# Kernel optimization log

Hardware: AMD Instinct MI355X
Metric: run time of the kernel (lower is better)

Reference implementation:

```python
import jax, jax.numpy as jnp
import numpy as np

N = 50000
E = 800000
G = 64
H, C = 16, 4  # heads, out_channels per head; H*C = 64


def setup_inputs() -> dict:
    key = jax.random.key(0)
    ks = jax.random.split(key, 16)
    return {
        "x": jax.random.normal(ks[0], (N,), jnp.float32),
        "edge_index": jax.random.randint(ks[1], (2, E), 0, N),
        "edge_attr": jax.random.normal(ks[2], (E,), jnp.float32),
        "batch": jnp.sort(jax.random.randint(ks[3], (N,), 0, G)),
        # GATv2Conv(1 -> 4, heads=16, edge_dim=1, concat=True)
        "Wl": jax.random.normal(ks[4], (1, H * C), jnp.float32) * 0.5,
        "bl": jnp.full((H * C,), 0.01, jnp.float32),
        "Wr": jax.random.normal(ks[5], (1, H * C), jnp.float32) * 0.5,
        "br": jnp.full((H * C,), 0.01, jnp.float32),
        "We": jax.random.normal(ks[6], (1, H * C), jnp.float32) * 0.5,
        "att": jax.random.normal(ks[7], (H, C), jnp.float32) * 0.5,
        "gat_bias": jnp.zeros((H * C,), jnp.float32),
        # GraphNorm(64)
        "gn_w": jnp.ones((H * C,), jnp.float32),
        "gn_b": jnp.zeros((H * C,), jnp.float32),
        "gn_ms": jnp.ones((H * C,), jnp.float32),
        # SAGEConv(64 -> 64, mean aggr, root weight)
        "sage_Wl": jax.random.normal(ks[8], (H * C, 64), jnp.float32) * 0.125,
        "sage_bl": jnp.full((64,), 0.01, jnp.float32),
        "sage_Wr": jax.random.normal(ks[9], (H * C, 64), jnp.float32) * 0.125,
        # MLP head
        "fc1_W": jax.random.normal(ks[10], (128, 2048), jnp.float32) * 0.08,
        "fc1_b": jnp.full((2048,), 0.01, jnp.float32),
        "fc2_W": jax.random.normal(ks[11], (2048, 1024), jnp.float32) * 0.02,
        "fc2_b": jnp.full((1024,), 0.01, jnp.float32),
        "fc3_W": jax.random.normal(ks[12], (1024, 3), jnp.float32) * 0.03,
        "fc3_b": jnp.full((3,), 0.01, jnp.float32),
    }


def reference(x, edge_index, edge_attr, batch, Wl, bl, Wr, br, We, att, gat_bias,
              gn_w, gn_b, gn_ms, sage_Wl, sage_bl, sage_Wr,
              fc1_W, fc1_b, fc2_W, fc2_b, fc3_W, fc3_b):
    src0, dst0 = edge_index[0], edge_index[1]
    x1 = x[:, None]  # [N,1] (torch.unsqueeze(x, -1))
    # ---- GATv2Conv ----
    xl = (x1 @ Wl + bl).reshape(N, H, C)  # source-side (x_j, also the value)
    xr = (x1 @ Wr + br).reshape(N, H, C)  # target-side (x_i)
    # add self loops; fill_value='mean' -> per-node mean of incoming edge_attr
    deg_in = jax.ops.segment_sum(jnp.ones((E,), x.dtype), dst0, num_segments=N)
    loop_attr = jax.ops.segment_sum(edge_attr, dst0, num_segments=N) / jnp.maximum(deg_in, 1.0)
    loops = jnp.arange(N)
    src = jnp.concatenate([src0, loops])
    dst = jnp.concatenate([dst0, loops])
    ea = jnp.concatenate([edge_attr, loop_attr])[:, None]  # [E+N,1]
    e = (ea @ We).reshape(-1, H, C)
    m = jax.nn.leaky_relu(xl[src] + xr[dst] + e, 0.2)  # [E+N,H,C]
    score = jnp.einsum('ehc,hc->eh', m, att)
    smax = jax.ops.segment_max(score, dst, num_segments=N)
    a = jnp.exp(score - smax[dst])
    denom = jax.ops.segment_sum(a, dst, num_segments=N)
    alpha = a / denom[dst]  # segmented softmax over incoming edges
    h = jax.ops.segment_sum(alpha[:, :, None] * xl[src], dst, num_segments=N)
    h = h.reshape(N, H * C) + gat_bias
    h = jax.nn.relu(h)
    # ---- GraphNorm ----
    cnt = jax.ops.segment_sum(jnp.ones((N,), x.dtype), batch, num_segments=G)[:, None]
    mean = jax.ops.segment_sum(h, batch, num_segments=G) / cnt
    o = h - mean[batch] * gn_ms
    var = jax.ops.segment_sum(o * o, batch, num_segments=G) / cnt
    h = gn_w * o / jnp.sqrt(var[batch] + 1e-5) + gn_b
    # ---- SAGEConv (mean aggregation + root weight) ----
    neigh = jax.ops.segment_sum(h[src0], dst0, num_segments=N) / jnp.maximum(deg_in, 1.0)[:, None]
    h = neigh @ sage_Wl + sage_bl + h @ sage_Wr
    h = jax.nn.relu(h)
    # ---- global max + mean pooling, MLP head (eval mode: dropout off) ----
    gmax = jax.ops.segment_max(h, batch, num_segments=G)
    gmean = jax.ops.segment_sum(h, batch, num_segments=G) / cnt
    g = jnp.concatenate([gmax, gmean], axis=1)  # [G, 128]
    g = jax.nn.relu(g @ fc1_W + fc1_b)
    g = jax.nn.relu(g @ fc2_W + fc2_b)
    return g @ fc3_W + fc3_b
```

## Files before the change

### kernel.cpp

```cpp
#include <hip/hip_runtime.h>

#define GG 64
#define HH 16
#define KK 64
#define S_SUB 8

__device__ __forceinline__ float bf2f(unsigned short u){
  return __uint_as_float(((unsigned)u) << 16);
}
__device__ __forceinline__ unsigned short f2bf(float f){
  unsigned u = __float_as_uint(f);
  unsigned r = u + 0x7fffu + ((u >> 16) & 1u);
  return (unsigned short)(r >> 16);
}

__global__ void k_zero(int4* __restrict__ p, int nInt4,
                       const int* __restrict__ batch, int N, int* __restrict__ goff){
  int t = blockIdx.x*blockDim.x + threadIdx.x;
  for (int i = t; i < nInt4; i += gridDim.x*blockDim.x)
    p[i] = make_int4(0,0,0,0);
  if (blockIdx.x == 0 && threadIdx.x <= GG){
    int g = threadIdx.x;
    int lo = 0, hi = N;
    while (lo < hi){ int mid = (lo+hi) >> 1; if (batch[mid] < g) lo = mid+1; else hi = mid; }
    goff[g] = lo;
  }
}


__global__ void k_count_rank(const int* __restrict__ ei, int* deg, int* __restrict__ rank, int E){
  int e = blockIdx.x*blockDim.x + threadIdx.x;
  if (e < E) rank[e] = atomicAdd(&deg[ei[E + e]], 1);
}

__global__ void k_scan1(const int* __restrict__ deg, int* __restrict__ bsum, int N){
  int base = blockIdx.x*1024;
  int lim = min(base + 1024, N);
  int s = 0;
  for (int i = base + (int)threadIdx.x; i < lim; i += 256) s += deg[i];
  #pragma unroll
  for (int ofs = 32; ofs >= 1; ofs >>= 1) s += __shfl_down(s, ofs, 64);
  __shared__ int ws[4];
  int lane = threadIdx.x & 63, wv = threadIdx.x >> 6;
  if (lane == 0) ws[wv] = s;
  __syncthreads();
  if (threadIdx.x == 0) bsum[blockIdx.x] = ws[0] + ws[1] + ws[2] + ws[3];
}

__global__ void __launch_bounds__(1024)
k_scan2(int* __restrict__ bsum, int* __restrict__ row_start_N, int NB){
  int t = threadIdx.x;
  int v = (t < NB) ? bsum[t] : 0;
  int lane = t & 63, wv = t >> 6;
  int val = v;
  #pragma unroll
  for (int ofs = 1; ofs < 64; ofs <<= 1){
    int tt = __shfl_up(val, ofs, 64);
    if (lane >= ofs) val += tt;
  }
  __shared__ int ws[16];
  if (lane == 63) ws[wv] = val;
  __syncthreads();
  if (t == 0){
    int run = 0;
    #pragma unroll
    for (int w = 0; w < 16; ++w){ int tmp = ws[w]; ws[w] = run; run += tmp; }
  }
  __syncthreads();
  int excl = ws[wv] + val - v;
  if (t < NB) bsum[t] = excl;
  if (t == NB - 1) *row_start_N = excl + v;
}

__global__ void k_scan3(const int* __restrict__ deg, const int* __restrict__ bsum,
                        int* __restrict__ row_start, int N){
  int b = blockIdx.x;
  int base = b*1024 + (int)threadIdx.x*4;
  int d0 = (base+0 < N) ? deg[base+0] : 0;
  int d1 = (base+1 < N) ? deg[base+1] : 0;
  int d2 = (base+2 < N) ? deg[base+2] : 0;
  int d3 = (base+3 < N) ? deg[base+3] : 0;
  int s = d0 + d1 + d2 + d3;
  int lane = threadIdx.x & 63, wv = threadIdx.x >> 6;
  int val = s;
  #pragma unroll
  for (int ofs = 1; ofs < 64; ofs <<= 1){
    int tt = __shfl_up(val, ofs, 64);
    if (lane >= ofs) val += tt;
  }
  __shared__ int ws[4];
  if (lane == 63) ws[wv] = val;
  __syncthreads();
  if (threadIdx.x == 0){
    int run = 0;
    #pragma unroll
    for (int w = 0; w < 4; ++w){ int tmp = ws[w]; ws[w] = run; run += tmp; }
  }
  __syncthreads();
  int pre = bsum[b] + ws[wv] + val - s;
  if (base+0 < N){ row_start[base+0] = pre; pre += d0; }
  if (base+1 < N){ row_start[base+1] = pre; pre += d1; }
  if (base+2 < N){ row_start[base+2] = pre; pre += d2; }
  if (base+3 < N){ row_start[base+3] = pre; }
}

__global__ void k_scatter(const int* __restrict__ ei, const float* __restrict__ ea,
                          const int* __restrict__ row_start, const int* __restrict__ rank,
                          int2* __restrict__ csr_se, int E){
  int e = blockIdx.x*blockDim.x + threadIdx.x;
  if (e >= E) return;
  int d = ei[E + e];
  int pos = row_start[d] + rank[e];
  csr_se[pos] = make_int2(ei[e], __float_as_int(ea[e]));
}

__global__ void k_gat(const float* __restrict__ x, const int* __restrict__ row_start,
                      const int2* __restrict__ cse,
                      const float* __restrict__ Wl, const float* __restrict__ bl,
                      const float* __restrict__ Wr, const float* __restrict__ br,
                      const float* __restrict__ We, const float* __restrict__ att,
                      const float* __restrict__ gat_bias,
                      float* __restrict__ h, int N){
  int t = blockIdx.x*blockDim.x + threadIdx.x;
  int n   = t >> 3;
  int sub = t & 7;
  if (n >= N) return;
  float xd = x[n];
  float wl[8], we[8], at[8], pre[8];
  int k0 = sub*8;
  #pragma unroll
  for (int i = 0; i < 8; ++i){
    int k = k0 + i;
    wl[i] = Wl[k]; we[i] = We[k]; at[i] = att[k];
    pre[i] = bl[k] + fmaf(xd, Wr[k], br[k]);
  }
  int e0 = row_start[n], e1 = row_start[n+1];
  float m[2]  = {-3.4e38f,-3.4e38f};
  float den[2] = {0,0}, S1[2] = {0,0};
  float asum = 0.f;

#define PROC(XS, EAV)                                                        \
  { float xs_ = (XS), ea_ = (EAV);                                           \
    _Pragma("unroll")                                                        \
    for (int hi2 = 0; hi2 < 2; ++hi2){                                       \
      float sc = 0.f;                                                        \
      _Pragma("unroll")                                                      \
      for (int c = 0; c < 4; ++c){                                           \
        int i = hi2*4 + c;                                                   \
        float tt = fmaf(xs_, wl[i], fmaf(ea_, we[i], pre[i]));               \
        tt = (tt > 0.f) ? tt : 0.2f*tt;                                      \
        sc = fmaf(tt, at[i], sc);                                            \
      }                                                                      \
      float nm = fmaxf(m[hi2], sc);                                          \
      float corr = __expf(m[hi2] - nm);                                      \
      float a    = __expf(sc - nm);                                          \
      den[hi2] = den[hi2]*corr + a;                                          \
      S1[hi2]  = S1[hi2] *corr + a*xs_;                                      \
      m[hi2] = nm; } }

  int e = e0;
  for (; e + 3 < e1; e += 4){
    int2 p0 = cse[e], p1 = cse[e+1], p2 = cse[e+2], p3 = cse[e+3];
    float xs0 = x[p0.x], xs1 = x[p1.x], xs2 = x[p2.x], xs3 = x[p3.x];
    float ea0 = __int_as_float(p0.y), ea1 = __int_as_float(p1.y);
    float ea2 = __int_as_float(p2.y), ea3 = __int_as_float(p3.y);
    asum += (ea0 + ea1) + (ea2 + ea3);
    PROC(xs0, ea0);
    PROC(xs1, ea1);
    PROC(xs2, ea2);
    PROC(xs3, ea3);
  }
  for (; e < e1; ++e){
    int2 p0 = cse[e];
    float xs0 = x[p0.x], ea0 = __int_as_float(p0.y);
    asum += ea0;
    PROC(xs0, ea0);
  }
  {
    float degf = (float)(e1 - e0);
    float eav = asum / fmaxf(degf, 1.0f);
    PROC(xd, eav);
  }
#undef PROC
  #pragma unroll
  for (int hi2 = 0; hi2 < 2; ++hi2){
    float r = S1[hi2] / den[hi2];
    float4 o;
    #pragma unroll
    for (int c = 0; c < 4; ++c){
      int i = hi2*4 + c, k = k0 + i;
      float v = fmaxf(fmaf(wl[i], r, bl[k] + gat_bias[k]), 0.f);
      ((float*)&o)[c] = v;
    }
    *(float4*)(h + (size_t)n*KK + k0 + hi2*4) = o;
  }
}

__global__ void k_gstats_part(const float* __restrict__ h, const int* __restrict__ goff,
                              float* __restrict__ gsum, float* __restrict__ gsum2){
  int g = blockIdx.x, sb = blockIdx.y;
  int s = goff[g], epos = goff[g+1];
  int k = threadIdx.x & 63, slice = threadIdx.x >> 6;
  float sum = 0.f, sum2 = 0.f;
  for (int n = s + sb*4 + slice; n < epos; n += S_SUB*4){
    float v = h[(size_t)n*KK + k];
    sum += v; sum2 += v*v;
  }
  __shared__ float ls[4][KK], ls2[4][KK];
  ls[slice][k] = sum; ls2[slice][k] = sum2;
  __syncthreads();
  if (slice == 0){
    float a  = ls[0][k]+ls[1][k]+ls[2][k]+ls[3][k];
    float b2 = ls2[0][k]+ls2[1][k]+ls2[2][k]+ls2[3][k];
    atomicAdd(&gsum[g*KK + k], a);
    atomicAdd(&gsum2[g*KK + k], b2);
  }
}

__global__ void k_norm(float* __restrict__ h, unsigned short* __restrict__ hb,
                       const int* __restrict__ batch,
                       const float* __restrict__ gsum, const float* __restrict__ gsum2,
                       const int* __restrict__ goff,
                       const float* __restrict__ gn_w, const float* __restrict__ gn_b,
                       const float* __restrict__ gn_ms, int N){
  int t = blockIdx.x*blockDim.x + threadIdx.x;
  if (t >= N*16) return;
  int n = t >> 4, q = t & 15;
  int b = batch[n];
  float c = fmaxf((float)(goff[b+1] - goff[b]), 1.0f);
  float inv = 1.0f / c;
  float4 hv = *(float4*)(h + (size_t)n*KK + q*4);
  float ov[4];
  #pragma unroll
  for (int i = 0; i < 4; ++i){
    int k = q*4 + i;
    float mean = gsum[b*KK + k]*inv;
    float eh2  = gsum2[b*KK + k]*inv;
    float ms = gn_ms[k];
    float var = eh2 - 2.f*ms*mean*mean + ms*ms*mean*mean;
    float sc = gn_w[k] * __frsqrt_rn(var + 1e-5f);
    float sh = gn_b[k] - sc*mean*ms;
    ov[i] = fmaf(sc, ((float*)&hv)[i], sh);
  }
  *(float4*)(h + (size_t)n*KK + q*4) = make_float4(ov[0], ov[1], ov[2], ov[3]);
  ushort4 bv;
  bv.x = f2bf(ov[0]); bv.y = f2bf(ov[1]); bv.z = f2bf(ov[2]); bv.w = f2bf(ov[3]);
  *(ushort4*)(hb + (size_t)n*KK + q*4) = bv;
}

__global__ void k_sage(const float* __restrict__ h, const unsigned short* __restrict__ hb,
                       const int* __restrict__ row_start, const int2* __restrict__ cse,
                       const float* __restrict__ Wl, const float* __restrict__ bln,
                       const float* __restrict__ Wr,
                       float* __restrict__ h2, int N){
  __shared__ float snm[16][KK], shn[16][KK];
  const ushort4* hb4 = (const ushort4*)hb;
  int tid = threadIdx.x;
  int u = tid >> 4;
  int q = tid & 15;
  int n = blockIdx.x*16 + u;
  if (n < N){
    int e0 = row_start[n], e1 = row_start[n+1];
    float a0=0.f,a1=0.f,a2=0.f,a3=0.f;
    float b0=0.f,b1=0.f,b2=0.f,b3=0.f;
    int e = e0;
    for (; e + 7 < e1; e += 8){
      int s0 = cse[e].x,   s1 = cse[e+1].x, s2 = cse[e+2].x, s3 = cse[e+3].x;
      int s4 = cse[e+4].x, s5 = cse[e+5].x, s6 = cse[e+6].x, s7 = cse[e+7].x;
      ushort4 v0 = hb4[(size_t)s0*16 + q];
      ushort4 v1 = hb4[(size_t)s1*16 + q];
      ushort4 v2 = hb4[(size_t)s2*16 + q];
      ushort4 v3 = hb4[(size_t)s3*16 + q];
      ushort4 v4 = hb4[(size_t)s4*16 + q];
      ushort4 v5 = hb4[(size_t)s5*16 + q];
      ushort4 v6 = hb4[(size_t)s6*16 + q];
      ushort4 v7 = hb4[(size_t)s7*16 + q];
      a0 += bf2f(v0.x); a1 += bf2f(v0.y); a2 += bf2f(v0.z); a3 += bf2f(v0.w);
      b0 += bf2f(v1.x); b1 += bf2f(v1.y); b2 += bf2f(v1.z); b3 += bf2f(v1.w);
      a0 += bf2f(v2.x); a1 += bf2f(v2.y); a2 += bf2f(v2.z); a3 += bf2f(v2.w);
      b0 += bf2f(v3.x); b1 += bf2f(v3.y); b2 += bf2f(v3.z); b3 += bf2f(v3.w);
      a0 += bf2f(v4.x); a1 += bf2f(v4.y); a2 += bf2f(v4.z); a3 += bf2f(v4.w);
      b0 += bf2f(v5.x); b1 += bf2f(v5.y); b2 += bf2f(v5.z); b3 += bf2f(v5.w);
      a0 += bf2f(v6.x); a1 += bf2f(v6.y); a2 += bf2f(v6.z); a3 += bf2f(v6.w);
      b0 += bf2f(v7.x); b1 += bf2f(v7.y); b2 += bf2f(v7.z); b3 += bf2f(v7.w);
    }
    if (e + 3 < e1){
      int s0 = cse[e].x, s1 = cse[e+1].x, s2 = cse[e+2].x, s3 = cse[e+3].x;
      ushort4 v0 = hb4[(size_t)s0*16 + q];
      ushort4 v1 = hb4[(size_t)s1*16 + q];
      ushort4 v2 = hb4[(size_t)s2*16 + q];
      ushort4 v3 = hb4[(size_t)s3*16 + q];
      a0 += bf2f(v0.x); a1 += bf2f(v0.y); a2 += bf2f(v0.z); a3 += bf2f(v0.w);
      b0 += bf2f(v1.x); b1 += bf2f(v1.y); b2 += bf2f(v1.z); b3 += bf2f(v1.w);
      a0 += bf2f(v2.x); a1 += bf2f(v2.y); a2 += bf2f(v2.z); a3 += bf2f(v2.w);
      b0 += bf2f(v3.x); b1 += bf2f(v3.y); b2 += bf2f(v3.z); b3 += bf2f(v3.w);
      e += 4;
    }
    for (; e < e1; ++e){
      ushort4 v0 = hb4[(size_t)cse[e].x*16 + q];
      a0 += bf2f(v0.x); a1 += bf2f(v0.y); a2 += bf2f(v0.z); a3 += bf2f(v0.w);
    }
    float dg = fmaxf((float)(e1 - e0), 1.0f);
    float inv = 1.0f/dg;
    float4 nm = make_float4((a0+b0)*inv, (a1+b1)*inv, (a2+b2)*inv, (a3+b3)*inv);
    *(float4*)&snm[u][q*4] = nm;
    *(float4*)&shn[u][q*4] = *(const float4*)(h + (size_t)n*KK + q*4);
  }
  __syncthreads();
  int j = tid & 63, u0 = tid >> 6;
  float acc[4];
  #pragma unroll
  for (int p = 0; p < 4; ++p) acc[p] = bln[j];
  for (int k = 0; k < KK; ++k){
    float wlv = Wl[k*KK + j], wrv = Wr[k*KK + j];
    #pragma unroll
    for (int p = 0; p < 4; ++p){
      int un = u0 + p*4;
      acc[p] = fmaf(snm[un][k], wlv, acc[p]);
      acc[p] = fmaf(shn[un][k], wrv, acc[p]);
    }
  }
  #pragma unroll
  for (int p = 0; p < 4; ++p){
    int un = u0 + p*4;
    int nn = blockIdx.x*16 + un;
    if (nn < N) h2[(size_t)nn*KK + j] = fmaxf(acc[p], 0.f);
  }
}

__global__ void k_pool_part(const float* __restrict__ h2, const int* __restrict__ goff,
                            unsigned* __restrict__ gmaxu, float* __restrict__ gsumP){
  int g = blockIdx.x, sb = blockIdx.y;
  int s = goff[g], epos = goff[g+1];
  int k = threadIdx.x & 63, slice = threadIdx.x >> 6;
  float mx = 0.f, sm = 0.f;
  for (int n = s + sb*4 + slice; n < epos; n += S_SUB*4){
    float v = h2[(size_t)n*KK + k];
    mx = fmaxf(mx, v); sm += v;
  }
  __shared__ float lm[4][KK], lsum[4][KK];
  lm[slice][k] = mx; lsum[slice][k] = sm;
  __syncthreads();
  if (slice == 0){
    float m2 = fmaxf(fmaxf(lm[0][k], lm[1][k]), fmaxf(lm[2][k], lm[3][k]));
    float s2 = lsum[0][k]+lsum[1][k]+lsum[2][k]+lsum[3][k];
    atomicMax(&gmaxu[g*KK + k], __float_as_uint(m2));
    atomicAdd(&gsumP[g*KK + k], s2);
  }
}


__global__ void k_fc1(const unsigned* __restrict__ gmaxu, const float* __restrict__ gsumP,
                      const int* __restrict__ goff,
                      const float* __restrict__ W, const float* __restrict__ b,
                      float* __restrict__ out){
  __shared__ float sin[128];
  int g = blockIdx.y, jt = blockIdx.x;
  int tid = threadIdx.x;
  if (tid < 128){
    float c = fmaxf((float)(goff[g+1] - goff[g]), 1.0f);
    sin[tid] = (tid < 64) ? __uint_as_float(gmaxu[g*64 + tid])
                          : gsumP[g*64 + (tid-64)] / c;
  }
  __syncthreads();
  int j = jt*256 + tid;
  float acc = b[j];
  #pragma unroll 16
  for (int k = 0; k < 128; ++k)
    acc = fmaf(sin[k], W[(size_t)k*2048 + j], acc);
  out[(size_t)g*2048 + j] = fmaxf(acc, 0.f);
}

__global__ void k_fc2a(const float* __restrict__ in, const float* __restrict__ W,
                       float* __restrict__ partial){
  __shared__ float sin[64][128];
  int jt = blockIdx.x, ks = blockIdx.y;
  int k0 = ks*128;
  int tid = threadIdx.x;
  for (int idx = tid; idx < 64*128; idx += 256){
    int g = idx >> 7, k = idx & 127;
    sin[g][k] = in[(size_t)g*2048 + k0 + k];
  }
  __syncthreads();
  int j = tid & 63, gs = tid >> 6;
  const float* Wp = W + (size_t)k0*1024 + jt*64 + j;
  float acc[16];
  #pragma unroll
  for (int p = 0; p < 16; ++p) acc[p] = 0.f;
  for (int k = 0; k < 128; ++k){
    float w = Wp[(size_t)k*1024];
    #pragma unroll
    for (int p = 0; p < 16; ++p)
      acc[p] = fmaf(sin[gs*16 + p][k], w, acc[p]);
  }
  #pragma unroll
  for (int p = 0; p < 16; ++p){
    int g = gs*16 + p;
    partial[((size_t)ks*64 + g)*1024 + jt*64 + j] = acc[p];
  }
}

__global__ void k_fc2red(const float* __restrict__ partial, const float* __restrict__ b,
                         float* __restrict__ out){
  int i = blockIdx.x*blockDim.x + threadIdx.x;
  int g = i >> 10, j = i & 1023;
  float s = b[j];
  #pragma unroll
  for (int ks = 0; ks < 16; ++ks)
    s += partial[((size_t)ks*64 + g)*1024 + j];
  out[i] = fmaxf(s, 0.f);
}

__global__ void k_fc3(const float* __restrict__ in, const float* __restrict__ W,
                      const float* __restrict__ b, float* __restrict__ out, int nOut){
  int w = (blockIdx.x*blockDim.x + threadIdx.x) >> 6;
  int lane = threadIdx.x & 63;
  if (w >= GG*nOut) return;
  int g = w / nOut, j = w - g*nOut;
  const float* row = in + (size_t)g*1024;
  float acc = 0.f;
  #pragma unroll
  for (int k = lane; k < 1024; k += 64)
    acc = fmaf(row[k], W[(size_t)k*nOut + j], acc);
  #pragma unroll
  for (int ofs = 32; ofs >= 1; ofs >>= 1)
    acc += __shfl_down(acc, ofs, 64);
  if (lane == 0) out[w] = acc + b[j];
}

extern "C" void kernel_launch(void* const* d_in, const int* in_sizes, int n_in,
                              void* d_out, int out_size, void* d_ws, size_t ws_size,
                              hipStream_t stream) {
  const float* x        = (const float*)d_in[0];
  const int*   ei       = (const int*)d_in[1];
  const float* ea       = (const float*)d_in[2];
  const int*   batch    = (const int*)d_in[3];
  const float* Wl       = (const float*)d_in[4];
  const float* bl       = (const float*)d_in[5];
  const float* Wr       = (const float*)d_in[6];
  const float* br       = (const float*)d_in[7];
  const float* We       = (const float*)d_in[8];
  const float* att      = (const float*)d_in[9];
  const float* gat_bias = (const float*)d_in[10];
  const float* gn_w     = (const float*)d_in[11];
  const float* gn_b     = (const float*)d_in[12];
  const float* gn_ms    = (const float*)d_in[13];
  const float* sage_Wl  = (const float*)d_in[14];
  const float* sage_bl  = (const float*)d_in[15];
  const float* sage_Wr  = (const float*)d_in[16];
  const float* fc1_W    = (const float*)d_in[17];
  const float* fc1_b    = (const float*)d_in[18];
  const float* fc2_W    = (const float*)d_in[19];
  const float* fc2_b    = (const float*)d_in[20];
  const float* fc3_W    = (const float*)d_in[21];
  const float* fc3_b    = (const float*)d_in[22];

  const int N = in_sizes[0];
  const int E = in_sizes[1] / 2;
  const int NB = (N + 1023) / 1024;

  char* ws = (char*)d_ws;
  size_t off = 0;
  auto alloc = [&](size_t bytes){ void* p = ws + off; off += (bytes + 255) & ~(size_t)255; return p; };

  int*      deg_i  = (int*)alloc((size_t)N*4);
  float*    gsum   = (float*)alloc(GG*KK*4);
  float*    gsum2  = (float*)alloc(GG*KK*4);
  unsigned* gmaxu  = (unsigned*)alloc(GG*KK*4);
  float*    gsumP  = (float*)alloc(GG*KK*4);
  size_t zero_bytes = off;
  int*   rank      = (int*)alloc((size_t)E*4);
  int*   bsum      = (int*)alloc((size_t)NB*4);
  int*   row_start = (int*)alloc((size_t)(N+1)*4);
  int*   goff      = (int*)alloc((GG+1)*4);
  int2*  csr_se    = (int2*)alloc((size_t)E*8);
  float* h         = (float*)alloc((size_t)N*KK*4);
  unsigned short* hb = (unsigned short*)alloc((size_t)N*KK*2);
  float* h2        = (float*)alloc((size_t)N*KK*4);
  float* out1      = (float*)alloc((size_t)GG*2048*4);
  float* out2      = (float*)alloc((size_t)GG*1024*4);
  float* partial   = (float*)alloc((size_t)16*GG*1024*4);
  (void)ws_size; (void)n_in; (void)out_size;

  const int B = 256;
  {
    int nInt4 = (int)(zero_bytes >> 4);
    int blocks = min((nInt4 + B - 1)/B, 256);
    k_zero <<<blocks, B, 0, stream>>>((int4*)d_ws, nInt4, batch, N, goff);
  }
  k_count_rank<<<(E+B-1)/B, B, 0, stream>>>(ei, deg_i, rank, E);
  k_scan1  <<<NB, B, 0, stream>>>(deg_i, bsum, N);
  k_scan2  <<<1, 1024, 0, stream>>>(bsum, row_start + N, NB);
  k_scan3  <<<NB, B, 0, stream>>>(deg_i, bsum, row_start, N);
  k_scatter<<<(E+B-1)/B, B, 0, stream>>>(ei, ea, row_start, rank, csr_se, E);
  k_gat    <<<((size_t)N*8+B-1)/B, B, 0, stream>>>(x, row_start, csr_se,
                                                   Wl, bl, Wr, br, We, att, gat_bias, h, N);
  {
    dim3 grid(GG, S_SUB);
    k_gstats_part<<<grid, 256, 0, stream>>>(h, goff, gsum, gsum2);
  }
  k_norm   <<<((size_t)N*16+B-1)/B, B, 0, stream>>>(h, hb, batch, gsum, gsum2, goff,
                                                    gn_w, gn_b, gn_ms, N);
  k_sage   <<<(N+15)/16, B, 0, stream>>>(h, hb, row_start, csr_se, sage_Wl, sage_bl, sage_Wr, h2, N);
  {
    dim3 grid(GG, S_SUB);
    k_pool_part<<<grid, 256, 0, stream>>>(h2, goff, gmaxu, gsumP);
  }
  {
    dim3 grid(8, GG);
    k_fc1  <<<grid, 256, 0, stream>>>(gmaxu, gsumP, goff, fc1_W, fc1_b, out1);
  }
  {
    dim3 grid(16, 16);
    k_fc2a <<<grid, 256, 0, stream>>>(out1, fc2_W, partial);
  }
  k_fc2red <<<(GG*1024+B-1)/B, B, 0, stream>>>(partial, fc2_b, out2);
  k_fc3    <<<(GG*3*64+B-1)/B, B, 0, stream>>>(out2, fc3_W, fc3_b, (float*)d_out, 3);
}
```

Measured before the change: 191.7 us.

## Fuse GraphNorm stats into GAT and pooling into SAGE; pack CSR entries

Computes the per-graph sum and sum-of-squares inside the GAT kernel through shared-memory run-length reduction and atomics, and computes max/mean pooling inside the SAGE kernel. This removes two separate kernels and the h2 buffer round-trip through global memory. It also packs the CSR source index (16 bits) and edge attribute (bf16) into one 32-bit word, halving the edge stream. The packing assumes N < 65536 and rounds edge_attr to bf16, which costs accuracy. The fused epilogues add more atomics per block.

After: 178.0 us. 7.1% less time.

```diff
diff --git a/kernel.cpp b/kernel.cpp
--- a/kernel.cpp
+++ b/kernel.cpp
@@ -3,7 +3,6 @@
 #define GG 64
 #define HH 16
 #define KK 64
-#define S_SUB 8
 
 __device__ __forceinline__ float bf2f(unsigned short u){
   return __uint_as_float(((unsigned)u) << 16);
@@ -106,115 +105,119 @@
 
 __global__ void k_scatter(const int* __restrict__ ei, const float* __restrict__ ea,
                           const int* __restrict__ row_start, const int* __restrict__ rank,
-                          int2* __restrict__ csr_se, int E){
+                          unsigned* __restrict__ cs, int E){
   int e = blockIdx.x*blockDim.x + threadIdx.x;
   if (e >= E) return;
   int d = ei[E + e];
   int pos = row_start[d] + rank[e];
-  csr_se[pos] = make_int2(ei[e], __float_as_int(ea[e]));
+  cs[pos] = ((unsigned)ei[e] & 0xFFFFu) | ((unsigned)f2bf(ea[e]) << 16);
 }
 
 __global__ void k_gat(const float* __restrict__ x, const int* __restrict__ row_start,
-                      const int2* __restrict__ cse,
+                      const unsigned* __restrict__ cs,
                       const float* __restrict__ Wl, const float* __restrict__ bl,
                       const float* __restrict__ Wr, const float* __restrict__ br,
                       const float* __restrict__ We, const float* __restrict__ att,
-                      const float* __restrict__ gat_bias,
-                      float* __restrict__ h, int N){
-  int t = blockIdx.x*blockDim.x + threadIdx.x;
+                      const float* __restrict__ gat_bias, const int* __restrict__ batch,
+                      float* __restrict__ h, float* __restrict__ gsum, float* __restrict__ gsum2,
+                      int N){
+  __shared__ float sh[32][KK+1];
+  __shared__ int bg[32];
+  int tid = threadIdx.x;
+  int t = blockIdx.x*blockDim.x + tid;
   int n   = t >> 3;
   int sub = t & 7;
-  if (n >= N) return;
-  float xd = x[n];
-  float wl[8], we[8], at[8], pre[8];
+  int u   = tid >> 3;
+  bool act = (n < N);
+  if (sub == 0) bg[u] = act ? batch[n] : -1;
   int k0 = sub*8;
-  #pragma unroll
-  for (int i = 0; i < 8; ++i){
-    int k = k0 + i;
-    wl[i] = Wl[k]; we[i] = We[k]; at[i] = att[k];
-    pre[i] = bl[k] + fmaf(xd, Wr[k], br[k]);
-  }
-  int e0 = row_start[n], e1 = row_start[n+1];
-  float m[2]  = {-3.4e38f,-3.4e38f};
-  float den[2] = {0,0}, S1[2] = {0,0};
-  float asum = 0.f;
+  if (act){
+    float xd = x[n];
+    float wl[8], we[8], at[8], pre[8];
+    #pragma unroll
+    for (int i = 0; i < 8; ++i){
+      int k = k0 + i;
+      wl[i] = Wl[k]; we[i] = We[k]; at[i] = att[k];
+      pre[i] = bl[k] + fmaf(xd, Wr[k], br[k]);
+    }
+    int e0 = row_start[n], e1 = row_start[n+1];
+    float m[2]  = {-3.4e38f,-3.4e38f};
+    float den[2] = {0,0}, S1[2] = {0,0};
+    float asum = 0.f;
 
 #define PROC(XS, EAV)                                                        \
-  { float xs_ = (XS), ea_ = (EAV);                                           \
-    _Pragma("unroll")                                                        \
-    for (int hi2 = 0; hi2 < 2; ++hi2){                                       \
-      float sc = 0.f;                                                        \
+    { float xs_ = (XS), ea_ = (EAV);                                         \
       _Pragma("unroll")                                                      \
-      for (int c = 0; c < 4; ++c){                                           \
-        int i = hi2*4 + c;                                                   \
-        float tt = fmaf(xs_, wl[i], fmaf(ea_, we[i], pre[i]));               \
-        tt = (tt > 0.f) ? tt : 0.2f*tt;                                      \
-        sc = fmaf(tt, at[i], sc);                                            \
-      }                                                                      \
-      float nm = fmaxf(m[hi2], sc);                                          \
-      float corr = __expf(m[hi2] - nm);                                      \
-      float a    = __expf(sc - nm);                                          \
-      den[hi2] = den[hi2]*corr + a;                                          \
-      S1[hi2]  = S1[hi2] *corr + a*xs_;                                      \
-      m[hi2] = nm; } }
-
-  int e = e0;
-  for (; e + 3 < e1; e += 4){
-    int2 p0 = cse[e], p1 = cse[e+1], p2 = cse[e+2], p3 = cse[e+3];
-    float xs0 = x[p0.x], xs1 = x[p1.x], xs2 = x[p2.x], xs3 = x[p3.x];
-    float ea0 = __int_as_float(p0.y), ea1 = __int_as_float(p1.y);
-    float ea2 = __int_as_float(p2.y), ea3 = __int_as_float(p3.y);
-    asum += (ea0 + ea1) + (ea2 + ea3);
-    PROC(xs0, ea0);
-    PROC(xs1, ea1);
-    PROC(xs2, ea2);
-    PROC(xs3, ea3);
-  }
-  for (; e < e1; ++e){
-    int2 p0 = cse[e];
-    float xs0 = x[p0.x], ea0 = __int_as_float(p0.y);
-    asum += ea0;
-    PROC(xs0, ea0);
-  }
-  {
-    float degf = (float)(e1 - e0);
-    float eav = asum / fmaxf(degf, 1.0f);
-    PROC(xd, eav);
-  }
+      for (int hi2 = 0; hi2 < 2; ++hi2){                                     \
+        float sc = 0.f;                                                      \
+        _Pragma("unroll")                                                    \
+        for (int c = 0; c < 4; ++c){                                         \
+          int i = hi2*4 + c;                                                 \
+          float tt = fmaf(xs_, wl[i], fmaf(ea_, we[i], pre[i]));             \
+          tt = (tt > 0.f) ? tt : 0.2f*tt;                                    \
+          sc = fmaf(tt, at[i], sc);                                          \
+        }                                                                    \
+        float nm = fmaxf(m[hi2], sc);                                        \
+        float corr = __expf(m[hi2] - nm);                                    \
+        float a    = __expf(sc - nm);                                        \
+        den[hi2] = den[hi2]*corr + a;                                        \
+        S1[hi2]  = S1[hi2] *corr + a*xs_;                                    \
+        m[hi2] = nm; } }
+
+    int e = e0;
+    for (; e + 3 < e1; e += 4){
+      unsigned w0 = cs[e], w1 = cs[e+1], w2 = cs[e+2], w3 = cs[e+3];
+      float xs0 = x[w0 & 0xFFFFu], xs1 = x[w1 & 0xFFFFu];
+      float xs2 = x[w2 & 0xFFFFu], xs3 = x[w3 & 0xFFFFu];
+      float ea0 = bf2f((unsigned short)(w0 >> 16)), ea1 = bf2f((unsigned short)(w1 >> 16));
+      float ea2 = bf2f((unsigned short)(w2 >> 16)), ea3 = bf2f((unsigned short)(w3 >> 16));
+      asum += (ea0 + ea1) + (ea2 + ea3);
+      PROC(xs0, ea0);
+      PROC(xs1, ea1);
+      PROC(xs2, ea2);
+      PROC(xs3, ea3);
+    }
+    for (; e < e1; ++e){
+      unsigned w0 = cs[e];
+      float xs0 = x[w0 & 0xFFFFu], ea0 = bf2f((unsigned short)(w0 >> 16));
+      asum += ea0;
+      PROC(xs0, ea0);
+    }
+    {
+      float degf = (float)(e1 - e0);
+      float eav = asum / fmaxf(degf, 1.0f);
+      PROC(xd, eav);
+    }
 #undef PROC
-  #pragma unroll
-  for (int hi2 = 0; hi2 < 2; ++hi2){
-    float r = S1[hi2] / den[hi2];
-    float4 o;
-    #pragma unroll
-    for (int c = 0; c < 4; ++c){
-      int i = hi2*4 + c, k = k0 + i;
-      float v = fmaxf(fmaf(wl[i], r, bl[k] + gat_bias[k]), 0.f);
-      ((float*)&o)[c] = v;
-    }
-    *(float4*)(h + (size_t)n*KK + k0 + hi2*4) = o;
-  }
-}
-
-__global__ void k_gstats_part(const float* __restrict__ h, const int* __restrict__ goff,
-                              float* __restrict__ gsum, float* __restrict__ gsum2){
-  int g = blockIdx.x, sb = blockIdx.y;
-  int s = goff[g], epos = goff[g+1];
-  int k = threadIdx.x & 63, slice = threadIdx.x >> 6;
-  float sum = 0.f, sum2 = 0.f;
-  for (int n = s + sb*4 + slice; n < epos; n += S_SUB*4){
-    float v = h[(size_t)n*KK + k];
-    sum += v; sum2 += v*v;
-  }
-  __shared__ float ls[4][KK], ls2[4][KK];
-  ls[slice][k] = sum; ls2[slice][k] = sum2;
-  __syncthreads();
-  if (slice == 0){
-    float a  = ls[0][k]+ls[1][k]+ls[2][k]+ls[3][k];
-    float b2 = ls2[0][k]+ls2[1][k]+ls2[2][k]+ls2[3][k];
-    atomicAdd(&gsum[g*KK + k], a);
-    atomicAdd(&gsum2[g*KK + k], b2);
-  }
+    #pragma unroll
+    for (int hi2 = 0; hi2 < 2; ++hi2){
+      float r = S1[hi2] / den[hi2];
+      float4 o;
+      #pragma unroll
+      for (int c = 0; c < 4; ++c){
+        int i = hi2*4 + c, k = k0 + i;
+        float v = fmaxf(fmaf(wl[i], r, bl[k] + gat_bias[k]), 0.f);
+        ((float*)&o)[c] = v;
+        sh[u][k] = v;
+      }
+      *(float4*)(h + (size_t)n*KK + k0 + hi2*4) = o;
+    }
+  } else {
+    #pragma unroll
+    for (int i = 0; i < 8; ++i) sh[u][k0+i] = 0.f;
+  }
+  __syncthreads();
+  int ch = tid & 63, slice = tid >> 6;
+  int cg = -2; float rs = 0.f, rs2 = 0.f;
+  for (int uu = slice*8; uu < slice*8 + 8; ++uu){
+    int g = bg[uu];
+    if (g != cg){
+      if (cg >= 0){ atomicAdd(&gsum[cg*KK + ch], rs); atomicAdd(&gsum2[cg*KK + ch], rs2); }
+      cg = g; rs = 0.f; rs2 = 0.f;
+    }
+    if (g >= 0){ float v = sh[uu][ch]; rs += v; rs2 += v*v; }
+  }
+  if (cg >= 0){ atomicAdd(&gsum[cg*KK + ch], rs); atomicAdd(&gsum2[cg*KK + ch], rs2); }
 }
 
 __global__ void k_norm(float* __restrict__ h, unsigned short* __restrict__ hb,
@@ -249,24 +252,26 @@
 }
 
 __global__ void k_sage(const float* __restrict__ h, const unsigned short* __restrict__ hb,
-                       const int* __restrict__ row_start, const int2* __restrict__ cse,
+                       const int* __restrict__ row_start, const unsigned* __restrict__ cs,
                        const float* __restrict__ Wl, const float* __restrict__ bln,
-                       const float* __restrict__ Wr,
-                       float* __restrict__ h2, int N){
+                       const float* __restrict__ Wr, const int* __restrict__ batch,
+                       unsigned* __restrict__ gmaxu, float* __restrict__ gsumP, int N){
   __shared__ float snm[16][KK], shn[16][KK];
+  __shared__ int bg[16];
   const ushort4* hb4 = (const ushort4*)hb;
   int tid = threadIdx.x;
   int u = tid >> 4;
   int q = tid & 15;
   int n = blockIdx.x*16 + u;
+  if (tid < 16) bg[tid] = (blockIdx.x*16 + tid < N) ? batch[blockIdx.x*16 + tid] : -1;
   if (n < N){
     int e0 = row_start[n], e1 = row_start[n+1];
     float a0=0.f,a1=0.f,a2=0.f,a3=0.f;
     float b0=0.f,b1=0.f,b2=0.f,b3=0.f;
     int e = e0;
     for (; e + 7 < e1; e += 8){
-      int s0 = cse[e].x,   s1 = cse[e+1].x, s2 = cse[e+2].x, s3 = cse[e+3].x;
-      int s4 = cse[e+4].x, s5 = cse[e+5].x, s6 = cse[e+6].x, s7 = cse[e+7].x;
+      int s0 = cs[e]   & 0xFFFF, s1 = cs[e+1] & 0xFFFF, s2 = cs[e+2] & 0xFFFF, s3 = cs[e+3] & 0xFFFF;
+      int s4 = cs[e+4] & 0xFFFF, s5 = cs[e+5] & 0xFFFF, s6 = cs[e+6] & 0xFFFF, s7 = cs[e+7] & 0xFFFF;
       ushort4 v0 = hb4[(size_t)s0*16 + q];
       ushort4 v1 = hb4[(size_t)s1*16 + q];
       ushort4 v2 = hb4[(size_t)s2*16 + q];
@@ -285,7 +290,7 @@
       b0 += bf2f(v7.x); b1 += bf2f(v7.y); b2 += bf2f(v7.z); b3 += bf2f(v7.w);
     }
     if (e + 3 < e1){
-      int s0 = cse[e].x, s1 = cse[e+1].x, s2 = cse[e+2].x, s3 = cse[e+3].x;
+      int s0 = cs[e] & 0xFFFF, s1 = cs[e+1] & 0xFFFF, s2 = cs[e+2] & 0xFFFF, s3 = cs[e+3] & 0xFFFF;
       ushort4 v0 = hb4[(size_t)s0*16 + q];
       ushort4 v1 = hb4[(size_t)s1*16 + q];
       ushort4 v2 = hb4[(size_t)s2*16 + q];
@@ -297,7 +302,7 @@
       e += 4;
     }
     for (; e < e1; ++e){
-      ushort4 v0 = hb4[(size_t)cse[e].x*16 + q];
+      ushort4 v0 = hb4[(size_t)(cs[e] & 0xFFFF)*16 + q];
       a0 += bf2f(v0.x); a1 += bf2f(v0.y); a2 += bf2f(v0.z); a3 += bf2f(v0.w);
     }
     float dg = fmaxf((float)(e1 - e0), 1.0f);
@@ -320,32 +325,28 @@
       acc[p] = fmaf(shn[un][k], wrv, acc[p]);
     }
   }
-  #pragma unroll
-  for (int p = 0; p < 4; ++p){
-    int un = u0 + p*4;
-    int nn = blockIdx.x*16 + un;
-    if (nn < N) h2[(size_t)nn*KK + j] = fmaxf(acc[p], 0.f);
-  }
-}
-
-__global__ void k_pool_part(const float* __restrict__ h2, const int* __restrict__ goff,
-                            unsigned* __restrict__ gmaxu, float* __restrict__ gsumP){
-  int g = blockIdx.x, sb = blockIdx.y;
-  int s = goff[g], epos = goff[g+1];
-  int k = threadIdx.x & 63, slice = threadIdx.x >> 6;
-  float mx = 0.f, sm = 0.f;
-  for (int n = s + sb*4 + slice; n < epos; n += S_SUB*4){
-    float v = h2[(size_t)n*KK + k];
-    mx = fmaxf(mx, v); sm += v;
-  }
-  __shared__ float lm[4][KK], lsum[4][KK];
-  lm[slice][k] = mx; lsum[slice][k] = sm;
-  __syncthreads();
-  if (slice == 0){
-    float m2 = fmaxf(fmaxf(lm[0][k], lm[1][k]), fmaxf(lm[2][k], lm[3][k]));
-    float s2 = lsum[0][k]+lsum[1][k]+lsum[2][k]+lsum[3][k];
-    atomicMax(&gmaxu[g*KK + k], __float_as_uint(m2));
-    atomicAdd(&gsumP[g*KK + k], s2);
+  __syncthreads();
+  #pragma unroll
+  for (int p = 0; p < 4; ++p)
+    snm[u0 + p*4][j] = fmaxf(acc[p], 0.f);
+  __syncthreads();
+  if (tid < 64){
+    int cg = -2; float rmax = 0.f, rsum = 0.f;
+    for (int uu = 0; uu < 16; ++uu){
+      int g = bg[uu];
+      if (g != cg){
+        if (cg >= 0){
+          atomicMax(&gmaxu[cg*KK + tid], __float_as_uint(rmax));
+          atomicAdd(&gsumP[cg*KK + tid], rsum);
+        }
+        cg = g; rmax = 0.f; rsum = 0.f;
+      }
+      if (g >= 0){ float v = snm[uu][tid]; rmax = fmaxf(rmax, v); rsum += v; }
+    }
+    if (cg >= 0){
+      atomicMax(&gmaxu[cg*KK + tid], __float_as_uint(rmax));
+      atomicAdd(&gsumP[cg*KK + tid], rsum);
+    }
   }
 }
 
@@ -473,10 +474,9 @@
   int*   bsum      = (int*)alloc((size_t)NB*4);
   int*   row_start = (int*)alloc((size_t)(N+1)*4);
   int*   goff      = (int*)alloc((GG+1)*4);
-  int2*  csr_se    = (int2*)alloc((size_t)E*8);
+  unsigned* csp    = (unsigned*)alloc((size_t)E*4);
   float* h         = (float*)alloc((size_t)N*KK*4);
   unsigned short* hb = (unsigned short*)alloc((size_t)N*KK*2);
-  float* h2        = (float*)alloc((size_t)N*KK*4);
   float* out1      = (float*)alloc((size_t)GG*2048*4);
   float* out2      = (float*)alloc((size_t)GG*1024*4);
   float* partial   = (float*)alloc((size_t)16*GG*1024*4);
@@ -492,20 +492,14 @@
   k_scan1  <<<NB, B, 0, stream>>>(deg_i, bsum, N);
   k_scan2  <<<1, 1024, 0, stream>>>(bsum, row_start + N, NB);
   k_scan3  <<<NB, B, 0, stream>>>(deg_i, bsum, row_start, N);
-  k_scatter<<<(E+B-1)/B, B, 0, stream>>>(ei, ea, row_start, rank, csr_se, E);
-  k_gat    <<<((size_t)N*8+B-1)/B, B, 0, stream>>>(x, row_start, csr_se,
-                                                   Wl, bl, Wr, br, We, att, gat_bias, h, N);
-  {
-    dim3 grid(GG, S_SUB);
-    k_gstats_part<<<grid, 256, 0, stream>>>(h, goff, gsum, gsum2);
-  }
+  k_scatter<<<(E+B-1)/B, B, 0, stream>>>(ei, ea, row_start, rank, csp, E);
+  k_gat    <<<((size_t)N*8+B-1)/B, B, 0, stream>>>(x, row_start, csp,
+                                                   Wl, bl, Wr, br, We, att, gat_bias,
+                                                   batch, h, gsum, gsum2, N);
   k_norm   <<<((size_t)N*16+B-1)/B, B, 0, stream>>>(h, hb, batch, gsum, gsum2, goff,
                                                     gn_w, gn_b, gn_ms, N);
-  k_sage   <<<(N+15)/16, B, 0, stream>>>(h, hb, row_start, csr_se, sage_Wl, sage_bl, sage_Wr, h2, N);
-  {
-    dim3 grid(GG, S_SUB);
-    k_pool_part<<<grid, 256, 0, stream>>>(h2, goff, gmaxu, gsumP);
-  }
+  k_sage   <<<(N+15)/16, B, 0, stream>>>(h, hb, row_start, csp, sage_Wl, sage_bl, sage_Wr,
+                                         batch, gmaxu, gsumP, N);
   {
     dim3 grid(8, GG);
     k_fc1  <<<grid, 256, 0, stream>>>(gmaxu, gsumP, goff, fc1_W, fc1_b, out1);
```
